# Performance work log

Hardware: AMD Instinct MI355X
Metric: run time of the kernel (lower is better)

## Reference

```python
import jax, jax.numpy as jnp
import numpy as np

F_DIM = 64; HID = 64; HEADS = 2; DH = 32; NG = 4; EPS = 1e-5; SCALE = 8.0  # sqrt(hid_dim)
B = 4; H = 64; W = 64; S = 8; CIN = 64


def _ln(x, g, b):
    mu = x.mean(-1, keepdims=True)
    var = ((x - mu) ** 2).mean(-1, keepdims=True)
    return (x - mu) * jax.lax.rsqrt(var + EPS) * g + b


def _gn(x, g, b):
    # x: [b, C, H, W]; normalize per group over (C/NG, H, W)
    bb, c, hh, ww = x.shape
    xg = x.reshape(bb, NG, -1)
    mu = xg.mean(-1, keepdims=True)
    var = ((xg - mu) ** 2).mean(-1, keepdims=True)
    xn = ((xg - mu) * jax.lax.rsqrt(var + EPS)).reshape(bb, c, hh, ww)
    return xn * g[None, :, None, None] + b[None, :, None, None]


def _mha(xq, xkv, qw, qb, kw, kb, vw, vb, ow, ob):
    # per-head attention with scaling by sqrt(hid_dim) (as in the source)
    q = xq @ qw + qb
    k = xkv @ kw + kb
    v = xkv @ vw + vb
    bb, l, _ = q.shape
    m = k.shape[1]
    qh = q.reshape(bb, l, HEADS, DH)
    kh = k.reshape(bb, m, HEADS, DH)
    vh = v.reshape(bb, m, HEADS, DH)
    s = jnp.einsum('blhd,bmhd->bhlm', qh, kh) / SCALE
    p = jax.nn.softmax(s, axis=-1)
    z = jnp.einsum('bhlm,bmhd->blhd', p, vh).reshape(bb, l, HID)
    return z @ ow + ob


def setup_inputs() -> dict:
    key = jax.random.key(0)
    ks = jax.random.split(key, 34)
    p = lambda k, shp: (jax.random.normal(k, shp, jnp.float32) * 0.02)
    d = {
        'x': jax.random.normal(ks[0], (B, H, W, F_DIM), jnp.float32),
        'slots': jax.random.normal(ks[1], (B, S, CIN), jnp.float32),
        'conv1_w': p(ks[2], (F_DIM, F_DIM)), 'conv1_b': p(ks[3], (F_DIM,)),
        'conv2_w': p(ks[4], (F_DIM, F_DIM)), 'conv2_b': p(ks[5], (F_DIM,)),
        'gn_g': jnp.ones((F_DIM,), jnp.float32), 'gn_b': jnp.zeros((F_DIM,), jnp.float32),
        'ln2_g': jnp.ones((F_DIM,), jnp.float32), 'ln2_b': jnp.zeros((F_DIM,), jnp.float32),
        'ln3_g': jnp.ones((F_DIM,), jnp.float32), 'ln3_b': jnp.zeros((F_DIM,), jnp.float32),
        'ln4_g': jnp.ones((F_DIM,), jnp.float32), 'ln4_b': jnp.zeros((F_DIM,), jnp.float32),
        'sa_qw': p(ks[6], (F_DIM, HID)), 'sa_qb': p(ks[7], (HID,)),
        'sa_kw': p(ks[8], (F_DIM, HID)), 'sa_kb': p(ks[9], (HID,)),
        'sa_vw': p(ks[10], (F_DIM, HID)), 'sa_vb': p(ks[11], (HID,)),
        'sa_ow': p(ks[12], (HID, F_DIM)), 'sa_ob': p(ks[13], (F_DIM,)),
        'ca_qw': p(ks[14], (F_DIM, HID)), 'ca_qb': p(ks[15], (HID,)),
        'ca_kw': p(ks[16], (CIN, HID)), 'ca_kb': p(ks[17], (HID,)),
        'ca_vw': p(ks[18], (CIN, HID)), 'ca_vb': p(ks[19], (HID,)),
        'ca_ow': p(ks[20], (HID, F_DIM)), 'ca_ob': p(ks[21], (F_DIM,)),
        'ff1_w': p(ks[22], (F_DIM, F_DIM)), 'ff1_b': p(ks[23], (F_DIM,)),
    }
    return d


def reference(x, slots, conv1_w, conv1_b, conv2_w, conv2_b, gn_g, gn_b,
              ln2_g, ln2_b, ln3_g, ln3_b, ln4_g, ln4_b,
              sa_qw, sa_qb, sa_kw, sa_kb, sa_vw, sa_vb, sa_ow, sa_ob,
              ca_qw, ca_qb, ca_kw, ca_kb, ca_vw, ca_vb, ca_ow, ca_ob,
              ff1_w, ff1_b):
    b, h, w, f = x.shape
    xc = jnp.transpose(x, (0, 3, 1, 2))               # [b,f,h,w]
    xc = _gn(xc, gn_g, gn_b)
    xc = jnp.einsum('bchw,oc->bohw', xc, conv1_w) + conv1_b[None, :, None, None]
    # faithful to torch: .contiguous().view(b,-1,f) on channels-first layout
    xs = xc.reshape(b, h * w, f)
    # repeat = 1
    xs = jax.nn.gelu(_ln(_mha(xs, xs, sa_qw, sa_qb, sa_kw, sa_kb, sa_vw, sa_vb, sa_ow, sa_ob), ln2_g, ln2_b) + xs, approximate=False)
    xs = _ln(_mha(xs, slots, ca_qw, ca_qb, ca_kw, ca_kb, ca_vw, ca_vb, ca_ow, ca_ob), ln3_g, ln3_b) + xs
    xs = _ln(xs @ ff1_w + ff1_b, ln4_g, ln4_b) + xs
    xo = jnp.transpose(xs.reshape(b, h, w, f), (0, 3, 1, 2))
    xo = jnp.einsum('bchw,oc->bohw', xo, conv2_w) + conv2_b[None, :, None, None]
    return jnp.transpose(xo, (0, 2, 3, 1))
```

## Files before the change

kernel.cpp:

```cpp
#include <hip/hip_runtime.h>
#include <hip/hip_bf16.h>
#include <math.h>

#define NBATCH 4
#define LTOK   4096
#define FD     64
#define KSPLIT 4
#define NIT    16

typedef __attribute__((ext_vector_type(8))) short short8v;
typedef __attribute__((ext_vector_type(4))) float f32x4;
typedef __attribute__((ext_vector_type(16))) float f32x16;

static __device__ inline uint32_t packbf2(float a, float b) {
    float2 f; f.x = a; f.y = b;
    __hip_bfloat162 h = __float22bfloat162_rn(f);
    uint32_t u; __builtin_memcpy(&u, &h, 4);
    return u;
}
static __device__ inline ushort packbf1(float a) {
    __hip_bfloat16 h = __float2bfloat16(a);
    ushort u; __builtin_memcpy(&u, &h, 2);
    return u;
}
static __device__ inline float gelu_exact(float y) {
    return 0.5f * y * (1.0f + erff(y * 0.70710678118654752f));
}

__global__ void gn_part_kernel(const float* __restrict__ x,
                               float* __restrict__ partS, float* __restrict__ partSS) {
    const int b = blockIdx.x >> 6, c = blockIdx.x & 63;
    const int t = threadIdx.x, l = t & 63, wv = t >> 6;
    const float4* xb = (const float4*)(x + (size_t)b * 262144) + (size_t)c * 1024;
    float s = 0.f, ss = 0.f;
#pragma unroll
    for (int k = 0; k < 4; k++) {
        float4 v = xb[t + 256 * k];
        s += (v.x + v.y) + (v.z + v.w);
        ss += (v.x * v.x + v.y * v.y) + (v.z * v.z + v.w * v.w);
    }
#pragma unroll
    for (int o = 0; o < 4; o++) {
        const int off = (int[]){1, 2, 16, 32}[o];
        s += __shfl_xor(s, off, 64);
        ss += __shfl_xor(ss, off, 64);
    }
    __shared__ float ls_s[4][4], ls_ss[4][4];
    if ((l & 51) == 0) { ls_s[wv][(l >> 2) & 3] = s; ls_ss[wv][(l >> 2) & 3] = ss; }
    __syncthreads();
    if (t < 4) {
        float S = 0.f, SS = 0.f;
#pragma unroll
        for (int w2 = 0; w2 < 4; w2++) { S += ls_s[w2][t]; SS += ls_ss[w2][t]; }
        partS[b * 256 + t * 64 + c] = S;
        partSS[b * 256 + t * 64 + c] = SS;
    }
}

__global__ void gn_conv1_kernel(const float* __restrict__ x,
                                const float* __restrict__ partS, const float* __restrict__ partSS,
                                const float* __restrict__ gg, const float* __restrict__ gb,
                                const float* __restrict__ w, const float* __restrict__ bias,
                                float* __restrict__ out) {
    const int b = blockIdx.x >> 6, i = blockIdx.x & 63;
    const int t = threadIdx.x;
    __shared__ float xn[64][65];
    __shared__ float wsm[64][64];
    __shared__ float sm[4], sr[4];
    {
        float sv = partS[b * 256 + t];
        float ssv = partSS[b * 256 + t];
        for (int o = 32; o; o >>= 1) { sv += __shfl_xor(sv, o, 64); ssv += __shfl_xor(ssv, o, 64); }
        if ((t & 63) == 0) {
            float mean = sv * (1.f / 65536.f);
            float var = ssv * (1.f / 65536.f) - mean * mean;
            sm[t >> 6] = mean;
            sr[t >> 6] = rsqrtf(var + 1e-5f);
        }
    }
    __syncthreads();
    {
        const int j = t >> 2, c0 = (t & 3) * 16, g = c0 >> 4;
        const float mean = sm[g], rstd = sr[g];
        const float* src = x + (((size_t)b * 64 + i) * 64 + j) * 64 + c0;
#pragma unroll
        for (int k = 0; k < 4; k++) {
            float4 v = *(const float4*)(src + 4 * k);
            xn[j][c0 + 4 * k + 0] = (v.x - mean) * rstd * gg[c0 + 4 * k + 0] + gb[c0 + 4 * k + 0];
            xn[j][c0 + 4 * k + 1] = (v.y - mean) * rstd * gg[c0 + 4 * k + 1] + gb[c0 + 4 * k + 1];
            xn[j][c0 + 4 * k + 2] = (v.z - mean) * rstd * gg[c0 + 4 * k + 2] + gb[c0 + 4 * k + 2];
            xn[j][c0 + 4 * k + 3] = (v.w - mean) * rstd * gg[c0 + 4 * k + 3] + gb[c0 + 4 * k + 3];
        }
        const int o = t >> 2, cc0 = (t & 3) * 16;
#pragma unroll
        for (int k = 0; k < 16; k++) wsm[cc0 + k][o] = w[o * 64 + cc0 + k];
    }
    __syncthreads();
    const int jj = t & 63, olo = (t >> 6) * 16;
    float acc[16];
#pragma unroll
    for (int oi = 0; oi < 16; oi++) acc[oi] = bias[olo + oi];
    for (int c = 0; c < 64; c++) {
        float xv = xn[jj][c];
#pragma unroll
        for (int oi = 0; oi < 16; oi++) acc[oi] += xv * wsm[c][olo + oi];
    }
#pragma unroll
    for (int oi = 0; oi < 16; oi++)
        out[((size_t)b * LTOK + (size_t)(olo + oi) * 64 + i) * 64 + jj] = acc[oi];
}

__global__ void qkv_kernel(const float* __restrict__ in,
                           const float* __restrict__ qw, const float* __restrict__ qb,
                           const float* __restrict__ kw, const float* __restrict__ kb,
                           const float* __restrict__ vw, const float* __restrict__ vb,
                           ushort* __restrict__ Qo, ushort* __restrict__ Ko, ushort* __restrict__ VTg) {
    __shared__ float xt[64][68];
    __shared__ float wt[64][64];
    __shared__ ushort vtr[64 * 72];
    const int t = threadIdx.x;
    const int ph = blockIdx.y;
    const size_t tok0 = (size_t)blockIdx.x * 64;
    const int b = blockIdx.x >> 6;
    const int tokb0 = (blockIdx.x & 63) * 64;
    const int r = t >> 2, cq = t & 3, olo = cq * 16;
    const float* W = (ph == 0) ? qw : (ph == 1) ? kw : vw;
    const float* Bb = (ph == 0) ? qb : (ph == 1) ? kb : vb;
    {
        const float4* src = (const float4*)(in + tok0 * 64) + (size_t)t * 4;
        float4* dst = (float4*)&xt[r][olo];
#pragma unroll
        for (int k = 0; k < 4; k++) dst[k] = src[k];
        const float4* ws2 = (const float4*)W + (size_t)t * 4;
        float4* wd = (float4*)wt + (size_t)t * 4;
#pragma unroll
        for (int k = 0; k < 4; k++) wd[k] = ws2[k];
    }
    __syncthreads();
    float acc[16];
#pragma unroll
    for (int k = 0; k < 4; k++) {
        float4 bv = *(const float4*)(Bb + olo + 4 * k);
        acc[4 * k] = bv.x; acc[4 * k + 1] = bv.y; acc[4 * k + 2] = bv.z; acc[4 * k + 3] = bv.w;
    }
    for (int f = 0; f < 64; f++) {
        float xv = xt[r][f];
#pragma unroll
        for (int oi = 0; oi < 16; oi++) acc[oi] += xv * wt[f][olo + oi];
    }
    if (ph < 2) {
        const float sc = (ph == 0) ? 0.180336880111f : 1.0f;
        uint32_t u[8];
#pragma unroll
        for (int i = 0; i < 8; i++) u[i] = packbf2(acc[2 * i] * sc, acc[2 * i + 1] * sc);
        ushort* op = (ph == 0 ? Qo : Ko) + (tok0 + r) * 64 + olo;
        *(uint4*)op = make_uint4(u[0], u[1], u[2], u[3]);
        *(uint4*)(op + 8) = make_uint4(u[4], u[5], u[6], u[7]);
    } else {
#pragma unroll
        for (int oi = 0; oi < 16; oi++) vtr[(olo + oi) * 72 + r] = packbf1(acc[oi]);
        __syncthreads();
        const int o = t >> 2, ch = t & 3;
        uint4 a0 = *(const uint4*)&vtr[o * 72 + ch * 16];
        uint4 a1 = *(const uint4*)&vtr[o * 72 + ch * 16 + 8];
        ushort* op = VTg + (size_t)(b * 64 + o) * 4096 + tokb0 + ch * 16;
        *(uint4*)op = a0;
        *(uint4*)(op + 8) = a1;
    }
}

__global__ __launch_bounds__(256) void flash_mfma(const ushort* __restrict__ Q,
                                                  const ushort* __restrict__ K,
                                                  const ushort* __restrict__ VTg,
                                                  float* __restrict__ Zp0, float* __restrict__ Zp1,
                                                  float* __restrict__ Zp2, float* __restrict__ Zp3,
                                                  float* __restrict__ Ls) {
    const int qt = blockIdx.x;
    const int bh = blockIdx.y;
    const int ks = blockIdx.z;
    const int b = bh >> 1, h = bh & 1;
    const int t = threadIdx.x;
    const int w = t >> 6, l = t & 63, lq = l & 31, sig = l >> 5;

    __shared__ ushort KsB[2][2048];
    __shared__ ushort VTB[2][2048];

    const size_t base = (size_t)b * LTOK * 64 + h * 32;
    const size_t vrow0 = (size_t)(b * 64 + h * 32);

    const int qrow = qt * 128 + w * 32 + lq;
    const short8v qf0 = *(const short8v*)(Q + base + (size_t)qrow * 64 + 8 * sig);
    const short8v qf1 = *(const short8v*)(Q + base + (size_t)qrow * 64 + 16 + 8 * sig);

    const int krow = t >> 2, kdg = t & 3;
    const int koff = ((krow << 5) + kdg * 8) ^ ((krow & 7) << 3);
    const int vrow = t >> 3, vc8 = t & 7;
    const int voff = ((vrow << 6) + vc8 * 8) ^ ((vrow & 7) << 3);
    const ushort* kgp = K + base + (size_t)(ks * NIT * 64 + krow) * 64 + kdg * 8;
    const ushort* vgp = VTg + (vrow0 + vrow) * 4096 + ks * NIT * 64 + vc8 * 8;

    *(uint4*)&KsB[0][koff] = *(const uint4*)kgp;  kgp += 64 * 64;
    *(uint4*)&VTB[0][voff] = *(const uint4*)vgp;  vgp += 64;

    f32x16 accZ;
#pragma unroll
    for (int i = 0; i < 16; i++) accZ[i] = 0.f;
    f32x16 zero16;
#pragma unroll
    for (int i = 0; i < 16; i++) zero16[i] = 0.f;
    float lacc = 0.0f;

    auto body = [&](const ushort* Kc, const ushort* Vc, ushort* Kn, ushort* Vn, bool pref) {
        __syncthreads();
        uint4 kq = make_uint4(0, 0, 0, 0), vq = make_uint4(0, 0, 0, 0);
        if (pref) {
            kq = *(const uint4*)kgp; kgp += 64 * 64;
            vq = *(const uint4*)vgp; vgp += 64;
        }
#pragma unroll
        for (int kb2 = 0; kb2 < 2; kb2++) {
            const int kb = kb2 * 32;
            const int kr = kb + lq;
            const short8v aK0 = *(const short8v*)&Kc[((kr << 5) + 8 * sig) ^ ((kr & 7) << 3)];
            const short8v aK1 = *(const short8v*)&Kc[((kr << 5) + 16 + 8 * sig) ^ ((kr & 7) << 3)];
            f32x16 st = __builtin_amdgcn_mfma_f32_32x32x16_bf16(aK0, qf0, zero16, 0, 0, 0);
            st = __builtin_amdgcn_mfma_f32_32x32x16_bf16(aK1, qf1, st, 0, 0, 0);
            uint32_t pk[8];
#pragma unroll
            for (int i = 0; i < 8; i++) {
                float p0 = __builtin_amdgcn_exp2f(st[2 * i]);
                float p1 = __builtin_amdgcn_exp2f(st[2 * i + 1]);
                lacc += p0 + p1;
                pk[i] = packbf2(p0, p1);
            }
            const uint32_t r1 = __shfl_xor(sig ? pk[0] : pk[2], 32, 64);
            const uint32_t r2 = __shfl_xor(sig ? pk[1] : pk[3], 32, 64);
            const uint32_t r3 = __shfl_xor(sig ? pk[4] : pk[6], 32, 64);
            const uint32_t r4 = __shfl_xor(sig ? pk[5] : pk[7], 32, 64);
            uint4 A0 = make_uint4(sig ? r1 : pk[0], sig ? r2 : pk[1],
                                  sig ? pk[2] : r1, sig ? pk[3] : r2);
            uint4 A1 = make_uint4(sig ? r3 : pk[4], sig ? r4 : pk[5],
                                  sig ? pk[6] : r3, sig ? pk[7] : r4);
            short8v aP0, aP1;
            __builtin_memcpy(&aP0, &A0, 16);
            __builtin_memcpy(&aP1, &A1, 16);
            const short8v vt0 = *(const short8v*)&Vc[((lq << 6) + kb + 8 * sig) ^ ((lq & 7) << 3)];
            const short8v vt1 = *(const short8v*)&Vc[((lq << 6) + kb + 16 + 8 * sig) ^ ((lq & 7) << 3)];
            accZ = __builtin_amdgcn_mfma_f32_32x32x16_bf16(aP0, vt0, accZ, 0, 0, 0);
            accZ = __builtin_amdgcn_mfma_f32_32x32x16_bf16(aP1, vt1, accZ, 0, 0, 0);
        }
        if (pref) {
            *(uint4*)&Kn[koff] = kq;
            *(uint4*)&Vn[voff] = vq;
        }
    };

#pragma unroll 1
    for (int it = 0; it < NIT / 2; it++) {
        body(KsB[0], VTB[0], KsB[1], VTB[1], true);
        body(KsB[1], VTB[1], KsB[0], VTB[0], it < NIT / 2 - 1);
    }

    float* Zo = (ks == 0) ? Zp0 : (ks == 1) ? Zp1 : (ks == 2) ? Zp2 : Zp3;
#pragma unroll
    for (int r = 0; r < 16; r++) {
        const int qr = qt * 128 + w * 32 + (r & 3) + 8 * (r >> 2) + 4 * sig;
        Zo[base + (size_t)qr * 64 + lq] = accZ[r];
    }
    lacc += __shfl_xor(lacc, 32, 64);
    if (l < 32)
        Ls[ks * 32768 + bh * 4096 + qt * 128 + w * 32 + lq] = lacc;
}

__global__ __launch_bounds__(256) void tail_fused(
    const float* __restrict__ Zp0, const float* __restrict__ Zp1,
    const float* __restrict__ Zp2, const float* __restrict__ Zp3,
    const float* __restrict__ Ls, const float* __restrict__ xs0,
    const float* __restrict__ slots,
    const float* __restrict__ ckw, const float* __restrict__ ckb,
    const float* __restrict__ cvw, const float* __restrict__ cvb,
    const float* __restrict__ ow, const float* __restrict__ ob,
    const float* __restrict__ g2, const float* __restrict__ b2,
    const float* __restrict__ qw, const float* __restrict__ qb,
    const float* __restrict__ cow, const float* __restrict__ cob,
    const float* __restrict__ g3, const float* __restrict__ b3,
    const float* __restrict__ fw, const float* __restrict__ fb,
    const float* __restrict__ g4, const float* __restrict__ b4,
    const float* __restrict__ cw, const float* __restrict__ cb,
    float* __restrict__ out)
{
    const int t = threadIdx.x;
    const size_t tok0 = (size_t)blockIdx.x * 32;
    const int b = blockIdx.x >> 7;
    const int r = t >> 3, c = t & 7, olo = c * 8;
    __shared__ float xt[32][68];
    __shared__ float wt[64][64];
    __shared__ float kcs[512], vcs[512], sls[512];

    float acc[8], res[8];

    auto stage_w = [&](const float* W) {
#pragma unroll
        for (int k = 0; k < 4; k++)
            ((float4*)wt)[4 * t + k] = ((const float4*)W)[4 * t + k];
    };
    auto stage_x_res = [&]() {
        float4* xd = (float4*)&xt[r][olo];
        xd[0] = make_float4(res[0], res[1], res[2], res[3]);
        xd[1] = make_float4(res[4], res[5], res[6], res[7]);
    };
    auto load8 = [&](float* dst, const float* p) {
        float4 u0 = *(const float4*)(p + olo);
        float4 u1 = *(const float4*)(p + olo + 4);
        dst[0] = u0.x; dst[1] = u0.y; dst[2] = u0.z; dst[3] = u0.w;
        dst[4] = u1.x; dst[5] = u1.y; dst[6] = u1.z; dst[7] = u1.w;
    };
    auto mm = [&](const float* bias) {
        load8(acc, bias);
        for (int f = 0; f < 64; f++) {
            float xv = xt[r][f];
#pragma unroll
            for (int oi = 0; oi < 8; oi++) acc[oi] += xv * wt[f][olo + oi];
        }
    };
    auto ln = [&](const float* gv, const float* bv, bool dogelu) {
        float s1 = 0.f, s2 = 0.f;
#pragma unroll
        for (int oi = 0; oi < 8; oi++) { s1 += acc[oi]; s2 += acc[oi] * acc[oi]; }
#pragma unroll
        for (int o = 1; o <= 4; o <<= 1) {
            s1 += __shfl_xor(s1, o, 64);
            s2 += __shfl_xor(s2, o, 64);
        }
        float mean = s1 * (1.f / 64.f);
        float var = s2 * (1.f / 64.f) - mean * mean;
        float rstd = rsqrtf(var + 1e-5f);
        float gl[8], bl[8];
        load8(gl, gv); load8(bl, bv);
#pragma unroll
        for (int oi = 0; oi < 8; oi++) {
            float y = (acc[oi] - mean) * rstd * gl[oi] + bl[oi] + res[oi];
            res[oi] = dogelu ? gelu_exact(y) : y;
        }
    };

    {
        if (t < 128) ((float4*)sls)[t] = ((const float4*)(slots + (size_t)b * 512))[t];
        const float4* z0 = (const float4*)(Zp0 + tok0 * 64);
        const float4* z1 = (const float4*)(Zp1 + tok0 * 64);
        const float4* z2 = (const float4*)(Zp2 + tok0 * 64);
        const float4* z3 = (const float4*)(Zp3 + tok0 * 64);
        float4 a0 = z0[2 * t], a1 = z0[2 * t + 1];
        float4 b0 = z1[2 * t], b1 = z1[2 * t + 1];
        float4 c0 = z2[2 * t], c1 = z2[2 * t + 1];
        float4 d0 = z3[2 * t], d1 = z3[2 * t + 1];
        const int hh = olo >> 5;
        const int bh_ = b * 2 + hh;
        const int tokb = (blockIdx.x & 127) * 32 + r;
        const float lt = Ls[bh_ * 4096 + tokb] + Ls[32768 + bh_ * 4096 + tokb]
                       + Ls[65536 + bh_ * 4096 + tokb] + Ls[98304 + bh_ * 4096 + tokb];
        const float inv = 1.0f / lt;
        float4* xd = (float4*)&xt[r][olo];
        xd[0] = make_float4(((a0.x + b0.x) + (c0.x + d0.x)) * inv,
                            ((a0.y + b0.y) + (c0.y + d0.y)) * inv,
                            ((a0.z + b0.z) + (c0.z + d0.z)) * inv,
                            ((a0.w + b0.w) + (c0.w + d0.w)) * inv);
        xd[1] = make_float4(((a1.x + b1.x) + (c1.x + d1.x)) * inv,
                            ((a1.y + b1.y) + (c1.y + d1.y)) * inv,
                            ((a1.z + b1.z) + (c1.z + d1.z)) * inv,
                            ((a1.w + b1.w) + (c1.w + d1.w)) * inv);
        stage_w(ow);
        float4 r0 = *(const float4*)(xs0 + (tok0 + r) * 64 + olo);
        float4 r1 = *(const float4*)(xs0 + (tok0 + r) * 64 + olo + 4);
        res[0] = r0.x; res[1] = r0.y; res[2] = r0.z; res[3] = r0.w;
        res[4] = r1.x; res[5] = r1.y; res[6] = r1.z; res[7] = r1.w;
    }
    __syncthreads();
    for (int jo = t; jo < 512; jo += 256) {
        const int j = jo >> 6, o = jo & 63;
        float ak = ckb[o], av = cvb[o];
#pragma unroll 8
        for (int c2 = 0; c2 < 64; c2++) {
            float sv = sls[j * 64 + c2];
            ak += sv * ckw[c2 * 64 + o];
            av += sv * cvw[c2 * 64 + o];
        }
        kcs[jo] = ak; vcs[jo] = av;
    }
    mm(ob);
    ln(g2, b2, true);

    __syncthreads();
    stage_x_res();
    stage_w(qw);
    __syncthreads();
    mm(qb);
    {
        float p[8];
        float mx = -3.0e38f;
#pragma unroll
        for (int j = 0; j < 8; j++) {
            float d = 0.f;
#pragma unroll
            for (int i2 = 0; i2 < 8; i2++) d += acc[i2] * kcs[j * 64 + olo + i2];
            d += __shfl_xor(d, 1, 64);
            d += __shfl_xor(d, 2, 64);
            d *= 0.125f;
            p[j] = d;
            mx = fmaxf(mx, d);
        }
        float es = 0.f;
#pragma unroll
        for (int j = 0; j < 8; j++) { p[j] = __expf(p[j] - mx); es += p[j]; }
        float inv = 1.f / es;
#pragma unroll
        for (int oi = 0; oi < 8; oi++) {
            float z = 0.f;
#pragma unroll
            for (int j = 0; j < 8; j++) z += p[j] * vcs[j * 64 + olo + oi];
            acc[oi] = z * inv;
        }
    }

    __syncthreads();
    {
        float4* xd = (float4*)&xt[r][olo];
        xd[0] = make_float4(acc[0], acc[1], acc[2], acc[3]);
        xd[1] = make_float4(acc[4], acc[5], acc[6], acc[7]);
    }
    stage_w(cow);
    __syncthreads();
    mm(cob);
    ln(g3, b3, false);

    __syncthreads();
    stage_x_res();
    stage_w(fw);
    __syncthreads();
    mm(fb);
    ln(g4, b4, false);

    __syncthreads();
    stage_x_res();
    {
        const int o5 = t >> 2, c5 = (t & 3) * 16;
#pragma unroll
        for (int k = 0; k < 16; k++) wt[c5 + k][o5] = cw[o5 * 64 + c5 + k];
    }
    __syncthreads();
    mm(cb);
    float* op = out + (tok0 + r) * 64 + olo;
    *(float4*)op = make_float4(acc[0], acc[1], acc[2], acc[3]);
    *(float4*)(op + 4) = make_float4(acc[4], acc[5], acc[6], acc[7]);
}

extern "C" void kernel_launch(void* const* d_in, const int* in_sizes, int n_in,
                              void* d_out, int out_size, void* d_ws, size_t ws_size,
                              hipStream_t stream) {
    const float* x       = (const float*)d_in[0];
    const float* slots   = (const float*)d_in[1];
    const float* conv1_w = (const float*)d_in[2];
    const float* conv1_b = (const float*)d_in[3];
    const float* conv2_w = (const float*)d_in[4];
    const float* conv2_b = (const float*)d_in[5];
    const float* gn_g    = (const float*)d_in[6];
    const float* gn_b    = (const float*)d_in[7];
    const float* ln2_g   = (const float*)d_in[8];
    const float* ln2_b   = (const float*)d_in[9];
    const float* ln3_g   = (const float*)d_in[10];
    const float* ln3_b   = (const float*)d_in[11];
    const float* ln4_g   = (const float*)d_in[12];
    const float* ln4_b   = (const float*)d_in[13];
    const float* sa_qw   = (const float*)d_in[14];
    const float* sa_qb   = (const float*)d_in[15];
    const float* sa_kw   = (const float*)d_in[16];
    const float* sa_kb   = (const float*)d_in[17];
    const float* sa_vw   = (const float*)d_in[18];
    const float* sa_vb   = (const float*)d_in[19];
    const float* sa_ow   = (const float*)d_in[20];
    const float* sa_ob   = (const float*)d_in[21];
    const float* ca_qw   = (const float*)d_in[22];
    const float* ca_qb   = (const float*)d_in[23];
    const float* ca_kw   = (const float*)d_in[24];
    const float* ca_kb   = (const float*)d_in[25];
    const float* ca_vw   = (const float*)d_in[26];
    const float* ca_vb   = (const float*)d_in[27];
    const float* ca_ow   = (const float*)d_in[28];
    const float* ca_ob   = (const float*)d_in[29];
    const float* ff1_w   = (const float*)d_in[30];
    const float* ff1_b   = (const float*)d_in[31];

    float* ws = (float*)d_ws;
    const size_t NBUF = (size_t)NBATCH * LTOK * FD;
    float* partS  = ws;
    float* partSS = ws + 1024;
    float* A      = ws + 4096;
    ushort* Kb    = (ushort*)(A + NBUF);
    ushort* VTgb  = Kb + NBUF;
    ushort* Qb    = VTgb + NBUF;
    float* Zp1    = (float*)(Qb + NBUF);
    float* Zp2    = Zp1 + NBUF;
    float* Zp3    = Zp2 + NBUF;
    float* Ls     = Zp3 + NBUF;
    float* Zp0    = (float*)d_out;

    gn_part_kernel<<<256, 256, 0, stream>>>(x, partS, partSS);
    gn_conv1_kernel<<<256, 256, 0, stream>>>(x, partS, partSS, gn_g, gn_b, conv1_w, conv1_b, A);
    qkv_kernel<<<dim3(256, 3), 256, 0, stream>>>(A, sa_qw, sa_qb, sa_kw, sa_kb, sa_vw, sa_vb, Qb, Kb, VTgb);
    flash_mfma<<<dim3(32, 8, KSPLIT), 256, 0, stream>>>(Qb, Kb, VTgb, Zp0, Zp1, Zp2, Zp3, Ls);
    tail_fused<<<512, 256, 0, stream>>>(Zp0, Zp1, Zp2, Zp3, Ls, A, slots,
                                        ca_kw, ca_kb, ca_vw, ca_vb,
                                        sa_ow, sa_ob, ln2_g, ln2_b,
                                        ca_qw, ca_qb, ca_ow, ca_ob, ln3_g, ln3_b,
                                        ff1_w, ff1_b, ln4_g, ln4_b,
                                        conv2_w, conv2_b, (float*)d_out);
}
```

Before: 94.54 us.

## Double key split, store bf16 partial attention outputs, use permlane32 swap

The flash attention kernel now splits the key range eight ways instead of four, giving twice as many workgroups each with half the iterations. Partial Z outputs are written as bf16 into one contiguous buffer instead of four fp32 buffers, so the tail kernel reads less data in a generic loop over splits. The shuffle-based lane exchange of the P fragments is replaced with v_permlane32_swap inline asm. Costs: more partial buffers for the tail to sum, and bf16 rounding of the partial sums reduces accuracy.

```diff
diff --git a/kernel.cpp b/kernel.cpp
--- a/kernel.cpp
+++ b/kernel.cpp
@@ -5,8 +5,8 @@
 #define NBATCH 4
 #define LTOK   4096
 #define FD     64
-#define KSPLIT 4
-#define NIT    16
+#define KSPLIT 8
+#define NIT    8
 
 typedef __attribute__((ext_vector_type(8))) short short8v;
 typedef __attribute__((ext_vector_type(4))) float f32x4;
@@ -172,8 +172,7 @@
 __global__ __launch_bounds__(256) void flash_mfma(const ushort* __restrict__ Q,
                                                   const ushort* __restrict__ K,
                                                   const ushort* __restrict__ VTg,
-                                                  float* __restrict__ Zp0, float* __restrict__ Zp1,
-                                                  float* __restrict__ Zp2, float* __restrict__ Zp3,
+                                                  ushort* __restrict__ ZpAll,
                                                   float* __restrict__ Ls) {
     const int qt = blockIdx.x;
     const int bh = blockIdx.y;
@@ -233,14 +232,16 @@
                 lacc += p0 + p1;
                 pk[i] = packbf2(p0, p1);
             }
-            const uint32_t r1 = __shfl_xor(sig ? pk[0] : pk[2], 32, 64);
-            const uint32_t r2 = __shfl_xor(sig ? pk[1] : pk[3], 32, 64);
-            const uint32_t r3 = __shfl_xor(sig ? pk[4] : pk[6], 32, 64);
-            const uint32_t r4 = __shfl_xor(sig ? pk[5] : pk[7], 32, 64);
-            uint4 A0 = make_uint4(sig ? r1 : pk[0], sig ? r2 : pk[1],
-                                  sig ? pk[2] : r1, sig ? pk[3] : r2);
-            uint4 A1 = make_uint4(sig ? r3 : pk[4], sig ? r4 : pk[5],
-                                  sig ? pk[6] : r3, sig ? pk[7] : r4);
+            uint32_t a0w0 = pk[0], a0w2 = pk[2];
+            uint32_t a0w1 = pk[1], a0w3 = pk[3];
+            uint32_t a1w0 = pk[4], a1w2 = pk[6];
+            uint32_t a1w1 = pk[5], a1w3 = pk[7];
+            asm volatile("v_permlane32_swap_b32 %0, %1" : "+v"(a0w0), "+v"(a0w2));
+            asm volatile("v_permlane32_swap_b32 %0, %1" : "+v"(a0w1), "+v"(a0w3));
+            asm volatile("v_permlane32_swap_b32 %0, %1" : "+v"(a1w0), "+v"(a1w2));
+            asm volatile("v_permlane32_swap_b32 %0, %1" : "+v"(a1w1), "+v"(a1w3));
+            uint4 A0 = make_uint4(a0w0, a0w1, a0w2, a0w3);
+            uint4 A1 = make_uint4(a1w0, a1w1, a1w2, a1w3);
             short8v aP0, aP1;
             __builtin_memcpy(&aP0, &A0, 16);
             __builtin_memcpy(&aP1, &A1, 16);
@@ -261,11 +262,11 @@
         body(KsB[1], VTB[1], KsB[0], VTB[0], it < NIT / 2 - 1);
     }
 
-    float* Zo = (ks == 0) ? Zp0 : (ks == 1) ? Zp1 : (ks == 2) ? Zp2 : Zp3;
+    ushort* Zo = ZpAll + (size_t)ks * (NBATCH * LTOK * FD);
 #pragma unroll
     for (int r = 0; r < 16; r++) {
         const int qr = qt * 128 + w * 32 + (r & 3) + 8 * (r >> 2) + 4 * sig;
-        Zo[base + (size_t)qr * 64 + lq] = accZ[r];
+        Zo[base + (size_t)qr * 64 + lq] = packbf1(accZ[r]);
     }
     lacc += __shfl_xor(lacc, 32, 64);
     if (l < 32)
@@ -273,8 +274,7 @@
 }
 
 __global__ __launch_bounds__(256) void tail_fused(
-    const float* __restrict__ Zp0, const float* __restrict__ Zp1,
-    const float* __restrict__ Zp2, const float* __restrict__ Zp3,
+    const ushort* __restrict__ ZpAll,
     const float* __restrict__ Ls, const float* __restrict__ xs0,
     const float* __restrict__ slots,
     const float* __restrict__ ckw, const float* __restrict__ ckb,
@@ -346,29 +346,30 @@
 
     {
         if (t < 128) ((float4*)sls)[t] = ((const float4*)(slots + (size_t)b * 512))[t];
-        const float4* z0 = (const float4*)(Zp0 + tok0 * 64);
-        const float4* z1 = (const float4*)(Zp1 + tok0 * 64);
-        const float4* z2 = (const float4*)(Zp2 + tok0 * 64);
-        const float4* z3 = (const float4*)(Zp3 + tok0 * 64);
-        float4 a0 = z0[2 * t], a1 = z0[2 * t + 1];
-        float4 b0 = z1[2 * t], b1 = z1[2 * t + 1];
-        float4 c0 = z2[2 * t], c1 = z2[2 * t + 1];
-        float4 d0 = z3[2 * t], d1 = z3[2 * t + 1];
+        float zs[8];
+#pragma unroll
+        for (int j = 0; j < 8; j++) zs[j] = 0.f;
+#pragma unroll
+        for (int kb = 0; kb < KSPLIT; kb++) {
+            const uint4 u = *(const uint4*)(ZpAll + (size_t)kb * (NBATCH * LTOK * FD)
+                                            + tok0 * 64 + (size_t)t * 8);
+            const uint32_t arr[4] = {u.x, u.y, u.z, u.w};
+#pragma unroll
+            for (int j = 0; j < 4; j++) {
+                zs[2 * j]     += __uint_as_float(arr[j] << 16);
+                zs[2 * j + 1] += __uint_as_float(arr[j] & 0xffff0000u);
+            }
+        }
         const int hh = olo >> 5;
         const int bh_ = b * 2 + hh;
         const int tokb = (blockIdx.x & 127) * 32 + r;
-        const float lt = Ls[bh_ * 4096 + tokb] + Ls[32768 + bh_ * 4096 + tokb]
-                       + Ls[65536 + bh_ * 4096 + tokb] + Ls[98304 + bh_ * 4096 + tokb];
+        float lt = 0.f;
+#pragma unroll
+        for (int kb = 0; kb < KSPLIT; kb++) lt += Ls[kb * 32768 + bh_ * 4096 + tokb];
         const float inv = 1.0f / lt;
         float4* xd = (float4*)&xt[r][olo];
-        xd[0] = make_float4(((a0.x + b0.x) + (c0.x + d0.x)) * inv,
-                            ((a0.y + b0.y) + (c0.y + d0.y)) * inv,
-                            ((a0.z + b0.z) + (c0.z + d0.z)) * inv,
-                            ((a0.w + b0.w) + (c0.w + d0.w)) * inv);
-        xd[1] = make_float4(((a1.x + b1.x) + (c1.x + d1.x)) * inv,
-                            ((a1.y + b1.y) + (c1.y + d1.y)) * inv,
-                            ((a1.z + b1.z) + (c1.z + d1.z)) * inv,
-                            ((a1.w + b1.w) + (c1.w + d1.w)) * inv);
+        xd[0] = make_float4(zs[0] * inv, zs[1] * inv, zs[2] * inv, zs[3] * inv);
+        xd[1] = make_float4(zs[4] * inv, zs[5] * inv, zs[6] * inv, zs[7] * inv);
         stage_w(ow);
         float4 r0 = *(const float4*)(xs0 + (tok0 + r) * 64 + olo);
         float4 r1 = *(const float4*)(xs0 + (tok0 + r) * 64 + olo + 4);
@@ -498,17 +499,14 @@
     ushort* Kb    = (ushort*)(A + NBUF);
     ushort* VTgb  = Kb + NBUF;
     ushort* Qb    = VTgb + NBUF;
-    float* Zp1    = (float*)(Qb + NBUF);
-    float* Zp2    = Zp1 + NBUF;
-    float* Zp3    = Zp2 + NBUF;
-    float* Ls     = Zp3 + NBUF;
-    float* Zp0    = (float*)d_out;
+    ushort* ZpAll = Qb + NBUF;
+    float* Ls     = (float*)(ZpAll + (size_t)KSPLIT * NBUF);
 
     gn_part_kernel<<<256, 256, 0, stream>>>(x, partS, partSS);
     gn_conv1_kernel<<<256, 256, 0, stream>>>(x, partS, partSS, gn_g, gn_b, conv1_w, conv1_b, A);
     qkv_kernel<<<dim3(256, 3), 256, 0, stream>>>(A, sa_qw, sa_qb, sa_kw, sa_kb, sa_vw, sa_vb, Qb, Kb, VTgb);
-    flash_mfma<<<dim3(32, 8, KSPLIT), 256, 0, stream>>>(Qb, Kb, VTgb, Zp0, Zp1, Zp2, Zp3, Ls);
-    tail_fused<<<512, 256, 0, stream>>>(Zp0, Zp1, Zp2, Zp3, Ls, A, slots,
+    flash_mfma<<<dim3(32, 8, KSPLIT), 256, 0, stream>>>(Qb, Kb, VTgb, ZpAll, Ls);
+    tail_fused<<<512, 256, 0, stream>>>(ZpAll, Ls, A, slots,
                                         ca_kw, ca_kb, ca_vw, ca_vb,
                                         sa_ow, sa_ob, ln2_g, ln2_b,
                                         ca_qw, ca_qb, ca_ow, ca_ob, ln3_g, ln3_b,
```

Result: faster. 90.85 us (-3.9%).
